# Performance work log

Hardware: AMD Instinct MI355X
Metric: run time of the kernel (lower is better)

## Reference

```python
import jax, jax.numpy as jnp
import numpy as np

N, E = 50000, 1600000
D_IN, D_OUT = 256, 64
ALPHA = 0.2        # LeakyReLU slope used on attention logits (self.leakyrelu)
BT_SLOPE = 0.01    # F.leaky_relu default slope inside relu_bt


def _xavier_normal(key, shape, gain):
    fan_in, fan_out = shape[0], shape[1]
    std = gain * np.sqrt(2.0 / (fan_in + fan_out))
    return jax.random.normal(key, shape, dtype=jnp.float32) * std


def relu_bt(x):
    # -threshold(-leaky_relu(x), -t, -t) == min(leaky_relu(x), t), t = ||x||_inf (detached)
    t = jax.lax.stop_gradient(jnp.max(jnp.abs(x)))
    y = jnp.where(x >= 0, x, BT_SLOPE * x)
    return jnp.minimum(y, t)


def setup_inputs() -> dict:
    key = jax.random.key(0)
    k0, k1, k2, k3, k4, k5 = jax.random.split(key, 6)
    inp = jax.random.normal(k0, (N, D_IN), dtype=jnp.float32)
    edge = jax.random.randint(k1, (2, E), 0, N, dtype=jnp.int64)
    W_high = _xavier_normal(k2, (D_IN, D_OUT), 1.414)
    W_low = _xavier_normal(k3, (D_IN, D_OUT), 1.414)
    a_high = _xavier_normal(k4, (1, D_OUT), 1.414)
    a_low = _xavier_normal(k5, (1, D_OUT), 1.414)
    return {"input": inp, "edge": edge, "W_high": W_high, "W_low": W_low,
            "a_high": a_high, "a_low": a_low}


def reference(input, edge, W_high, W_low, a_high, a_low):
    n = input.shape[0]
    src, dst = edge[0], edge[1]

    h_high = relu_bt(input @ W_high)  # [N, D_OUT]
    h_low = relu_bt(input @ W_low)    # [N, D_OUT]

    # a @ (h[src] -/+ h[dst])^T == (a.h)[src] -/+ (a.h)[dst]: compute per-node scalar
    # projections first, then gather scalars per edge (avoids [E, D_OUT] edge features).
    s_high = h_high @ a_high[0]       # [N]
    s_low = h_low @ a_low[0]          # [N]

    def lrelu(x):
        return jnp.where(x >= 0, x, ALPHA * x)

    edge_e_high = jnp.exp(-lrelu(s_high[src] - s_high[dst]))  # [E]
    edge_e_low = jnp.exp(-lrelu(s_low[src] + s_low[dst]))     # [E]
    # dropout p=0.0 -> identity

    # sparse A @ ones -> per-row sum of attention weights
    rowsum_high = jax.ops.segment_sum(edge_e_high, src, num_segments=n)[:, None]
    rowsum_low = jax.ops.segment_sum(edge_e_low, src, num_segments=n)[:, None]

    # sparse A @ h -> weighted aggregation of neighbor features
    hp_high = jax.ops.segment_sum(edge_e_high[:, None] * h_high[dst], src, num_segments=n)
    hp_low = jax.ops.segment_sum(edge_e_low[:, None] * h_low[dst], src, num_segments=n)

    hp_high = hp_high / (rowsum_high + 1e-16)
    hp_low = hp_low / (rowsum_low + 1e-16)

    # concat=True branch
    return relu_bt(jnp.concatenate([hp_high, hp_low], axis=1))  # [N, 2*D_OUT]
```

## Files before the change

### kernel.cpp

```cpp
#include <hip/hip_runtime.h>
#include <hip/hip_bf16.h>
#include <cstdint>

#define NN    50000
#define NE    1600000
#define DIN   256
#define DOUT  64
#define CAPS  96
#define CAPD  95

#define BKT   196
#define BCAP  10240
#define EPB   4096
#define EPT   16
#define NBIN  391
#define MTB   64
#define NGEMM 782

typedef __attribute__((ext_vector_type(8))) short frag8;
typedef __attribute__((ext_vector_type(4))) float fragc;

union PK { __hip_bfloat162 b2; uint32_t u; };
union CH { frag8 v; uint32_t u[4]; };

__device__ __forceinline__ float leaky01(float x) { return x >= 0.f ? x : 0.01f * x; }

__device__ __forceinline__ uint32_t pk2(float lo, float hi) {
  PK p; p.b2 = __float22bfloat162_rn(make_float2(lo, hi)); return p.u;
}

__device__ __forceinline__ int   bcast_i(int v, int lane) {
  return __builtin_amdgcn_readlane(v, lane);
}

__device__ __forceinline__ float bfH(uint32_t u) { return __uint_as_float(u << 16); }
__device__ __forceinline__ float bfL(uint32_t u) { return __uint_as_float(u & 0xffff0000u); }

__global__ __launch_bounds__(256) void prep_kernel(
    const float* __restrict__ Wh, const float* __restrict__ Wl,
    __hip_bfloat16* __restrict__ Wt, int* __restrict__ cursor)
{
  if (blockIdx.x == 0 && threadIdx.x < BKT) cursor[threadIdx.x] = 0;
  int g = blockIdx.x * 256 + threadIdx.x;
  if (g < 2 * DOUT * DIN) {
    int m = g >> 14, rem = g & 16383;
    int n = rem >> 8, k = rem & 255;
    float v = (m ? Wl : Wh)[k * DOUT + n];
    Wt[g] = __float2bfloat16(v);
  }
}

__global__ __launch_bounds__(256) void fused_kernel(
    const float* __restrict__ inp, const __hip_bfloat16* __restrict__ Wt,
    const float* __restrict__ ah, const float* __restrict__ al,
    const int* __restrict__ edge, int* __restrict__ cursor,
    uint32_t* __restrict__ binned, uint32_t* __restrict__ HL,
    float2* __restrict__ ss)
{
  __shared__ __align__(16) char smem[32768];

  const int idx = blockIdx.x;
  const int t = threadIdx.x;

  if (idx < NBIN) {
    uint32_t* stage  = (uint32_t*)smem;
    int*      hist   = (int*)(smem + 16384);
    int*      cur    = (int*)(smem + 17408);
    int*      base_g = (int*)(smem + 18192);
    int*      scan_s = (int*)(smem + 18976);

    const int e0 = idx * EPB;
    uint32_t v[EPT];
#pragma unroll
    for (int i = 0; i < EPT; i++) {
      int e = e0 + i * 256 + t;
      if (e < NE) {
        uint32_t s = (uint32_t)edge[e];
        uint32_t d = (uint32_t)edge[NE + e];
        v[i] = (s << 16) | d;
      } else {
        v[i] = 0xFFFFFFFFu;
      }
    }
    if (t < 256) hist[t] = 0;
    for (int b = t; b < BKT; b += 256) cur[b] = 0;
    __syncthreads();
#pragma unroll
    for (int i = 0; i < EPT; i++) {
      int b = v[i] >> 24;
      if (b < BKT) atomicAdd(&hist[b], 1);
    }
    __syncthreads();
    if (t < 64) {
      int carry = 0;
#pragma unroll
      for (int seg = 0; seg < 4; seg++) {
        int i = seg * 64 + t;
        int h = hist[i];
        int s = h;
#pragma unroll
        for (int off = 1; off < 64; off <<= 1) {
          int o = __shfl_up(s, off);
          if (t >= off) s += o;
        }
        int excl = carry + s - h;
        if (i <= BKT) scan_s[i] = excl;
        carry += bcast_i(s, 63);
      }
    }
    __syncthreads();
    for (int b = t; b < BKT; b += 256) {
      int h = hist[b];
      base_g[b] = h ? atomicAdd(&cursor[b], h) : 0;
    }
    __syncthreads();
#pragma unroll
    for (int i = 0; i < EPT; i++) {
      int b = v[i] >> 24;
      if (b < BKT) {
        int pos = atomicAdd(&cur[b], 1);
        stage[scan_s[b] + pos] = v[i];
      }
    }
    __syncthreads();
    const int total = scan_s[BKT];
    for (int i = t; i < total; i += 256) {
      uint32_t sv = stage[i];
      int bb = sv >> 24;
      int ofs = base_g[bb] + (i - scan_s[bb]);
      if (ofs < BCAP) binned[(size_t)bb * BCAP + ofs] = sv;
    }
    return;
  }

  const int gid = idx - NBIN;
  const int n0 = gid * MTB;
  const int lane = t & 63;
  const int w = t >> 6;
  const int quad = lane >> 4, nn = lane & 15;

  const frag8* Wt8 = (const frag8*)Wt;
  const int bbase = ((w * 16 + nn) << 5) + quad;
  frag8 bH[8], bL[8];
#pragma unroll
  for (int q = 0; q < 8; q++) {
    bH[q] = Wt8[bbase + (q << 2)];
    bL[q] = Wt8[2048 + bbase + (q << 2)];
  }

  const float4* inp4 = (const float4*)inp;
  const int l5 = t & 31;
  const int rw = t >> 5;
  {
    const int q8 = l5 >> 2, qd = l5 & 3;
#pragma unroll
    for (int i = 0; i < 8; i++) {
      int row = i * 8 + rw;
      int node = n0 + row;
      float4 a0 = make_float4(0.f, 0.f, 0.f, 0.f), a1 = a0;
      if (node < NN) {
        a0 = inp4[(size_t)node * 64 + l5 * 2];
        a1 = inp4[(size_t)node * 64 + l5 * 2 + 1];
      }
      int c = ((row >> 4) << 9) | (q8 << 6) | (qd << 4) | (row & 15);
      int B = c << 4;
      B ^= ((B >> 8) & 7) << 4;
      CH ch;
      ch.u[0] = pk2(a0.x, a0.y);
      ch.u[1] = pk2(a0.z, a0.w);
      ch.u[2] = pk2(a1.x, a1.y);
      ch.u[3] = pk2(a1.z, a1.w);
      *(frag8*)(smem + B) = ch.v;
    }
  }
  __syncthreads();

  fragc accH[4], accL[4];
#pragma unroll
  for (int m = 0; m < 4; m++) {
    accH[m] = (fragc){0.f, 0.f, 0.f, 0.f};
    accL[m] = (fragc){0.f, 0.f, 0.f, 0.f};
  }

#pragma unroll
  for (int q = 0; q < 8; q++) {
#pragma unroll
    for (int mt = 0; mt < 4; mt++) {
      int R = (mt << 13) + (q << 10) + (lane << 4);
      R ^= ((R >> 8) & 7) << 4;
      frag8 af = *(const frag8*)(smem + R);
      accH[mt] = __builtin_amdgcn_mfma_f32_16x16x32_bf16(af, bH[q], accH[mt], 0, 0, 0);
      accL[mt] = __builtin_amdgcn_mfma_f32_16x16x32_bf16(af, bL[q], accL[mt], 0, 0, 0);
    }
  }
  __syncthreads();

  float* sred = (float*)smem;
  const float ahv = ah[w * 16 + nn];
  const float alv = al[w * 16 + nn];
#pragma unroll
  for (int mt = 0; mt < 4; mt++) {
#pragma unroll
    for (int r = 0; r < 4; r++) {
      int rowb = (mt << 4) + (quad << 2) + r;
      int node = n0 + rowb;
      float hH = leaky01(accH[mt][r]);
      float hL = leaky01(accL[mt][r]);
      if (node < NN) HL[(size_t)node * DOUT + w * 16 + nn] = pk2(hH, hL);
      float pH = hH * ahv, pL = hL * alv;
#pragma unroll
      for (int off = 1; off < 16; off <<= 1) {
        pH += __shfl_xor(pH, off);
        pL += __shfl_xor(pL, off);
      }
      if (nn == 0) {
        sred[rowb * 8 + w]     = pH;
        sred[rowb * 8 + 4 + w] = pL;
      }
    }
  }
  __syncthreads();
  if (t < 64) {
    int node = n0 + t;
    if (node < NN) {
      float sH = sred[t * 8 + 0] + sred[t * 8 + 1] + sred[t * 8 + 2] + sred[t * 8 + 3];
      float sL = sred[t * 8 + 4] + sred[t * 8 + 5] + sred[t * 8 + 6] + sred[t * 8 + 7];
      ss[node] = make_float2(sH, sL);
    }
  }
}

__global__ __launch_bounds__(256) void csr_kernel(
    const uint32_t* __restrict__ binned, const int* __restrict__ cursor,
    unsigned short* __restrict__ col)
{
  __shared__ __align__(16) unsigned short lst[64][CAPS];
  __shared__ int cnt[64];
  const int blk = blockIdx.x;
  const int b    = ((blk >> 5) << 3) + (blk & 7);
  const int part = (blk >> 3) & 3;
  if (b >= BKT) return;
  const int t = threadIdx.x;
  if (t < 64) cnt[t] = 0;
  __syncthreads();
  int n = cursor[b]; if (n > BCAP) n = BCAP;
  const uint32_t* eb = binned + (size_t)b * BCAP;
  for (int i = t; i < n; i += 256) {
    uint32_t v = eb[i];
    int src = v >> 16, dst = v & 0xffff;
    int loc = src & 255;
    if ((loc >> 6) == part) {
      int pos = atomicAdd(&cnt[loc & 63], 1);
      if (pos < CAPD) lst[loc & 63][1 + pos] = (unsigned short)dst;
    }
  }
  __syncthreads();
  if (t < 64) {
    int c = cnt[t]; if (c > CAPD) c = CAPD;
    lst[t][0] = (unsigned short)c;
  }
  __syncthreads();
  const int base_node = (b << 8) + (part << 6);
  int4* dst4 = (int4*)(col + (size_t)base_node * CAPS);
  const int4* src4 = (const int4*)&lst[0][0];
  for (int i = t; i < 64 * CAPS / 8; i += 256) {
    int node = base_node + i / (CAPS / 8);
    if (node < NN) dst4[i] = src4[i];
  }
}

__global__ __launch_bounds__(256) void agg_kernel(
    const uint32_t* __restrict__ HL, const float2* __restrict__ ss,
    const unsigned short* __restrict__ col, float* __restrict__ out)
{
  int wave = (blockIdx.x * blockDim.x + threadIdx.x) >> 6;
  int lane = threadIdx.x & 63;
  if (wave >= NN) return;
  const int n = wave;
  const unsigned short* cl = col + (size_t)n * CAPS;
  int d = cl[0]; if (d > CAPD) d = CAPD;

  const float2 sn = ss[n];
  const uint2* HL2 = (const uint2*)HL;

  const int vodd4 = (lane & 32) >> 3;
  const int lo31  = lane & 31;

  float accH0 = 0.f, accH1 = 0.f, accL0 = 0.f, accL1 = 0.f;
  float rsH = 0.f, rsL = 0.f;

  for (int base = 0; base < d; base += 64) {
    int m = d - base; if (m > 64) m = 64;
    int   dst_l = 0;
    float eh_l = 0.f, el_l = 0.f;
    if (lane < m) {
      dst_l = cl[1 + base + lane];
      float2 sd = ss[dst_l];
      float xh = sn.x - sd.x;
      xh = (xh >= 0.f) ? xh : 0.2f * xh;
      eh_l = __expf(-xh);
      float xl = sn.y + sd.y;
      xl = (xl >= 0.f) ? xl : 0.2f * xl;
      el_l = __expf(-xl);
    }
    const int ehb = __float_as_int(eh_l);
    const int elb = __float_as_int(el_l);
    const int pj = (m + 1) >> 1;
    for (int jj = 0; jj < pj; jj += 4) {
      int vdd[4]; float veh[4], vel[4]; uint2 u[4];
#pragma unroll
      for (int x = 0; x < 4; x++) {
        int ib = vodd4 + ((jj + x) << 3);
        vdd[x] = __builtin_amdgcn_ds_bpermute(ib, dst_l);
        veh[x] = __int_as_float(__builtin_amdgcn_ds_bpermute(ib, ehb));
        vel[x] = __int_as_float(__builtin_amdgcn_ds_bpermute(ib, elb));
      }
#pragma unroll
      for (int x = 0; x < 4; x++)
        u[x] = HL2[(((uint32_t)vdd[x]) << 5) + lo31];
#pragma unroll
      for (int x = 0; x < 4; x++) {
        accH0 += veh[x] * bfH(u[x].x);
        accL0 += vel[x] * bfL(u[x].x);
        accH1 += veh[x] * bfH(u[x].y);
        accL1 += vel[x] * bfL(u[x].y);
      }
    }
    float rh = eh_l, rl = el_l;
#pragma unroll
    for (int off = 1; off < 64; off <<= 1) {
      rh += __shfl_xor(rh, off);
      rl += __shfl_xor(rl, off);
    }
    rsH += rh; rsL += rl;
  }

  accH0 += __shfl_xor(accH0, 32);
  accH1 += __shfl_xor(accH1, 32);
  accL0 += __shfl_xor(accL0, 32);
  accL1 += __shfl_xor(accL1, 32);

  float r  = (lane < 32) ? rsH : rsL;
  float a0 = (lane < 32) ? accH0 : accL0;
  float a1 = (lane < 32) ? accH1 : accL1;
  float inv = 1.f / (r + 1e-16f);
  float o0 = leaky01(a0 * inv);
  float o1 = leaky01(a1 * inv);
  float2* op = (float2*)(out + (size_t)n * 128 + ((lane & 32) << 1) + (lo31 << 1));
  *op = make_float2(o0, o1);
}

extern "C" void kernel_launch(void* const* d_in, const int* in_sizes, int n_in,
                              void* d_out, int out_size, void* d_ws, size_t ws_size,
                              hipStream_t stream) {
  const float* inp  = (const float*)d_in[0];
  const int*   edge = (const int*)d_in[1];
  const float* Wh   = (const float*)d_in[2];
  const float* Wl   = (const float*)d_in[3];
  const float* ah   = (const float*)d_in[4];
  const float* al   = (const float*)d_in[5];
  float* out = (float*)d_out;

  char* ws = (char*)d_ws;
  uint32_t* HL     = (uint32_t*)(ws + 0);
  float2*   ss     = (float2*)  (ws + 12800000);
  unsigned short* col = (unsigned short*)(ws + 13200000);
  uint32_t* binned = (uint32_t*)(ws + 32400000);
  int*      cursor = (int*)     (ws + 40428160);
  __hip_bfloat16* Wt = (__hip_bfloat16*)(ws + 13200000);

  prep_kernel<<<128, 256, 0, stream>>>(Wh, Wl, Wt, cursor);
  fused_kernel<<<NBIN + NGEMM, 256, 0, stream>>>(inp, Wt, ah, al, edge,
                                                 cursor, binned, HL, ss);
  csr_kernel<<<800, 256, 0, stream>>>(binned, cursor, col);
  agg_kernel<<<NN / 4, 256, 0, stream>>>(HL, ss, col, out);
}
```

Baseline: 193.7 us.

## Split edge binning into own kernel and co-schedule CSR build with GEMM

Edge binning moves out of the fused GEMM kernel into a standalone bin kernel with smaller per-block chunks (2048 edges, twice as many blocks). The CSR construction blocks are then merged into the GEMM launch, so the node-projection GEMM overlaps with CSR building rather than with binning. The Wt buffer is moved to its own workspace region because it was previously aliased with the col buffer that CSR now writes concurrently. This keeps the same number of launches, but binning now runs alone, and smaller bins mean more global cursor atomics.

Result: slower. 204.6 us (+5.6%).

```diff
diff --git a/kernel.cpp b/kernel.cpp
--- a/kernel.cpp
+++ b/kernel.cpp
@@ -11,11 +11,12 @@
 
 #define BKT   196
 #define BCAP  10240
-#define EPB   4096
-#define EPT   16
-#define NBIN  391
+#define EPB   2048
+#define EPT   8
+#define NBIN  782
 #define MTB   64
 #define NGEMM 782
+#define NCSR  800
 
 typedef __attribute__((ext_vector_type(8))) short frag8;
 typedef __attribute__((ext_vector_type(4))) float fragc;
@@ -50,11 +51,86 @@
   }
 }
 
-__global__ __launch_bounds__(256) void fused_kernel(
+__global__ __launch_bounds__(256) void bin_kernel(
+    const int* __restrict__ edge, int* __restrict__ cursor,
+    uint32_t* __restrict__ binned)
+{
+  __shared__ __align__(16) char smem[11584];
+  uint32_t* stage  = (uint32_t*)smem;
+  int*      hist   = (int*)(smem + 8192);
+  int*      cur    = (int*)(smem + 9216);
+  int*      base_g = (int*)(smem + 10000);
+  int*      scan_s = (int*)(smem + 10784);
+
+  const int t = threadIdx.x;
+  const int e0 = blockIdx.x * EPB;
+  uint32_t v[EPT];
+#pragma unroll
+  for (int i = 0; i < EPT; i++) {
+    int e = e0 + i * 256 + t;
+    if (e < NE) {
+      uint32_t s = (uint32_t)edge[e];
+      uint32_t d = (uint32_t)edge[NE + e];
+      v[i] = (s << 16) | d;
+    } else {
+      v[i] = 0xFFFFFFFFu;
+    }
+  }
+  hist[t] = 0;
+  for (int b = t; b < BKT; b += 256) cur[b] = 0;
+  __syncthreads();
+#pragma unroll
+  for (int i = 0; i < EPT; i++) {
+    int b = v[i] >> 24;
+    if (b < BKT) atomicAdd(&hist[b], 1);
+  }
+  __syncthreads();
+  if (t < 64) {
+    int carry = 0;
+#pragma unroll
+    for (int seg = 0; seg < 4; seg++) {
+      int i = seg * 64 + t;
+      int h = hist[i];
+      int s = h;
+#pragma unroll
+      for (int off = 1; off < 64; off <<= 1) {
+        int o = __shfl_up(s, off);
+        if (t >= off) s += o;
+      }
+      int excl = carry + s - h;
+      if (i <= BKT) scan_s[i] = excl;
+      carry += bcast_i(s, 63);
+    }
+  }
+  __syncthreads();
+  for (int b = t; b < BKT; b += 256) {
+    int h = hist[b];
+    base_g[b] = h ? atomicAdd(&cursor[b], h) : 0;
+  }
+  __syncthreads();
+#pragma unroll
+  for (int i = 0; i < EPT; i++) {
+    int b = v[i] >> 24;
+    if (b < BKT) {
+      int pos = atomicAdd(&cur[b], 1);
+      stage[scan_s[b] + pos] = v[i];
+    }
+  }
+  __syncthreads();
+  const int total = scan_s[BKT];
+  for (int i = t; i < total; i += 256) {
+    uint32_t sv = stage[i];
+    int bb = sv >> 24;
+    int ofs = base_g[bb] + (i - scan_s[bb]);
+    if (ofs < BCAP) binned[(size_t)bb * BCAP + ofs] = sv;
+  }
+}
+
+__global__ __launch_bounds__(256) void gemcsr_kernel(
     const float* __restrict__ inp, const __hip_bfloat16* __restrict__ Wt,
     const float* __restrict__ ah, const float* __restrict__ al,
-    const int* __restrict__ edge, int* __restrict__ cursor,
-    uint32_t* __restrict__ binned, uint32_t* __restrict__ HL,
+    const uint32_t* __restrict__ binned, const int* __restrict__ cursor,
+    unsigned short* __restrict__ col, uint32_t* __restrict__ HL,
     float2* __restrict__ ss)
 {
   __shared__ __align__(16) char smem[32768];
@@ -62,79 +138,43 @@
   const int idx = blockIdx.x;
   const int t = threadIdx.x;
 
-  if (idx < NBIN) {
-    uint32_t* stage  = (uint32_t*)smem;
-    int*      hist   = (int*)(smem + 16384);
-    int*      cur    = (int*)(smem + 17408);
-    int*      base_g = (int*)(smem + 18192);
-    int*      scan_s = (int*)(smem + 18976);
-
-    const int e0 = idx * EPB;
-    uint32_t v[EPT];
-#pragma unroll
-    for (int i = 0; i < EPT; i++) {
-      int e = e0 + i * 256 + t;
-      if (e < NE) {
-        uint32_t s = (uint32_t)edge[e];
-        uint32_t d = (uint32_t)edge[NE + e];
-        v[i] = (s << 16) | d;
-      } else {
-        v[i] = 0xFFFFFFFFu;
-      }
-    }
-    if (t < 256) hist[t] = 0;
-    for (int b = t; b < BKT; b += 256) cur[b] = 0;
+  if (idx >= NGEMM) {
+    unsigned short (*lst)[CAPS] = (unsigned short (*)[CAPS])smem;
+    int* cnt = (int*)(smem + 12288);
+    const int cIdx = idx - NGEMM;
+    const int b    = ((cIdx >> 5) << 3) + (cIdx & 7);
+    const int part = (cIdx >> 3) & 3;
+    if (b >= BKT) return;
+    if (t < 64) cnt[t] = 0;
     __syncthreads();
-#pragma unroll
-    for (int i = 0; i < EPT; i++) {
-      int b = v[i] >> 24;
-      if (b < BKT) atomicAdd(&hist[b], 1);
+    int n = cursor[b]; if (n > BCAP) n = BCAP;
+    const uint32_t* eb = binned + (size_t)b * BCAP;
+    for (int i = t; i < n; i += 256) {
+      uint32_t v = eb[i];
+      int src = v >> 16, dst = v & 0xffff;
+      int loc = src & 255;
+      if ((loc >> 6) == part) {
+        int pos = atomicAdd(&cnt[loc & 63], 1);
+        if (pos < CAPD) lst[loc & 63][1 + pos] = (unsigned short)dst;
+      }
     }
     __syncthreads();
     if (t < 64) {
-      int carry = 0;
-#pragma unroll
-      for (int seg = 0; seg < 4; seg++) {
-        int i = seg * 64 + t;
-        int h = hist[i];
-        int s = h;
-#pragma unroll
-        for (int off = 1; off < 64; off <<= 1) {
-          int o = __shfl_up(s, off);
-          if (t >= off) s += o;
-        }
-        int excl = carry + s - h;
-        if (i <= BKT) scan_s[i] = excl;
-        carry += bcast_i(s, 63);
-      }
+      int c = cnt[t]; if (c > CAPD) c = CAPD;
+      lst[t][0] = (unsigned short)c;
     }
     __syncthreads();
-    for (int b = t; b < BKT; b += 256) {
-      int h = hist[b];
-      base_g[b] = h ? atomicAdd(&cursor[b], h) : 0;
-    }
-    __syncthreads();
-#pragma unroll
-    for (int i = 0; i < EPT; i++) {
-      int b = v[i] >> 24;
-      if (b < BKT) {
-        int pos = atomicAdd(&cur[b], 1);
-        stage[scan_s[b] + pos] = v[i];
-      }
-    }
-    __syncthreads();
-    const int total = scan_s[BKT];
-    for (int i = t; i < total; i += 256) {
-      uint32_t sv = stage[i];
-      int bb = sv >> 24;
-      int ofs = base_g[bb] + (i - scan_s[bb]);
-      if (ofs < BCAP) binned[(size_t)bb * BCAP + ofs] = sv;
+    const int base_node = (b << 8) + (part << 6);
+    int4* dst4 = (int4*)(col + (size_t)base_node * CAPS);
+    const int4* src4 = (const int4*)&lst[0][0];
+    for (int i = t; i < 64 * CAPS / 8; i += 256) {
+      int node = base_node + i / (CAPS / 8);
+      if (node < NN) dst4[i] = src4[i];
     }
     return;
   }
 
-  const int gid = idx - NBIN;
-  const int n0 = gid * MTB;
+  const int n0 = idx * MTB;
   const int lane = t & 63;
   const int w = t >> 6;
   const int quad = lane >> 4, nn = lane & 15;
@@ -227,45 +267,6 @@
       float sL = sred[t * 8 + 4] + sred[t * 8 + 5] + sred[t * 8 + 6] + sred[t * 8 + 7];
       ss[node] = make_float2(sH, sL);
     }
-  }
-}
-
-__global__ __launch_bounds__(256) void csr_kernel(
-    const uint32_t* __restrict__ binned, const int* __restrict__ cursor,
-    unsigned short* __restrict__ col)
-{
-  __shared__ __align__(16) unsigned short lst[64][CAPS];
-  __shared__ int cnt[64];
-  const int blk = blockIdx.x;
-  const int b    = ((blk >> 5) << 3) + (blk & 7);
-  const int part = (blk >> 3) & 3;
-  if (b >= BKT) return;
-  const int t = threadIdx.x;
-  if (t < 64) cnt[t] = 0;
-  __syncthreads();
-  int n = cursor[b]; if (n > BCAP) n = BCAP;
-  const uint32_t* eb = binned + (size_t)b * BCAP;
-  for (int i = t; i < n; i += 256) {
-    uint32_t v = eb[i];
-    int src = v >> 16, dst = v & 0xffff;
-    int loc = src & 255;
-    if ((loc >> 6) == part) {
-      int pos = atomicAdd(&cnt[loc & 63], 1);
-      if (pos < CAPD) lst[loc & 63][1 + pos] = (unsigned short)dst;
-    }
-  }
-  __syncthreads();
-  if (t < 64) {
-    int c = cnt[t]; if (c > CAPD) c = CAPD;
-    lst[t][0] = (unsigned short)c;
-  }
-  __syncthreads();
-  const int base_node = (b << 8) + (part << 6);
-  int4* dst4 = (int4*)(col + (size_t)base_node * CAPS);
-  const int4* src4 = (const int4*)&lst[0][0];
-  for (int i = t; i < 64 * CAPS / 8; i += 256) {
-    int node = base_node + i / (CAPS / 8);
-    if (node < NN) dst4[i] = src4[i];
   }
 }
 
@@ -365,13 +366,13 @@
   uint32_t* HL     = (uint32_t*)(ws + 0);
   float2*   ss     = (float2*)  (ws + 12800000);
   unsigned short* col = (unsigned short*)(ws + 13200000);
+  __hip_bfloat16* Wt  = (__hip_bfloat16*)(ws + 24000000);
   uint32_t* binned = (uint32_t*)(ws + 32400000);
   int*      cursor = (int*)     (ws + 40428160);
-  __hip_bfloat16* Wt = (__hip_bfloat16*)(ws + 13200000);
 
   prep_kernel<<<128, 256, 0, stream>>>(Wh, Wl, Wt, cursor);
-  fused_kernel<<<NBIN + NGEMM, 256, 0, stream>>>(inp, Wt, ah, al, edge,
-                                                 cursor, binned, HL, ss);
-  csr_kernel<<<800, 256, 0, stream>>>(binned, cursor, col);
+  bin_kernel<<<NBIN, 256, 0, stream>>>(edge, cursor, binned);
+  gemcsr_kernel<<<NGEMM + NCSR, 256, 0, stream>>>(inp, Wt, ah, al, binned,
+                                                  cursor, col, HL, ss);
   agg_kernel<<<NN / 4, 256, 0, stream>>>(HL, ss, col, out);
 }
```
